# Performance work log

Measured on AMD Instinct MI355X. Metric: run time of the kernel, lower is better.

Reference implementation:

```python
import jax, jax.numpy as jnp
import numpy as np


def setup_inputs() -> dict:
    key = jax.random.key(0)
    ks = jax.random.split(key, 8)
    B, C, N = 2, 128, 8192
    E, NNZ = 1024, 4096
    return {
        "vertex_feat": jax.random.normal(ks[0], (B, C, N), dtype=jnp.float32),
        "edge_feat": jax.random.normal(ks[1], (B, C, E), dtype=jnp.float32),
        "edge_weight": jax.random.uniform(ks[2], (E,), dtype=jnp.float32),
        "incidence": jax.random.randint(ks[3], (2, NNZ), 0, E, dtype=jnp.int64),
        "inv_edge_degree": jax.random.uniform(ks[4], (E,), dtype=jnp.float32),
        "inv_vertex_degree": jax.random.uniform(ks[5], (N,), dtype=jnp.float32),
        "edge_scale": jnp.ones((1,), dtype=jnp.float32),
        "knn_k": 20,
    }


def _knn_edge_aggregate(vertex_feat, knn_k):
    # vertex_feat: [B, C, N]
    B, C, N = vertex_feat.shape
    x = vertex_feat
    xx = jnp.sum(x * x, axis=1)                      # [B, N]
    inner = -2.0 * jnp.einsum("bcn,bcm->bnm", x, x)  # [B, N, N]
    dist = xx[:, :, None] + inner + xx[:, None, :]    # [B, N, N]
    # topk of -dist, drop self (nearest)
    _, idx = jax.lax.top_k(-dist, knn_k + 1)          # [B, N, k+1]
    idx = idx[:, :, 1:]                               # [B, N, k]
    vf = jnp.transpose(x, (0, 2, 1))                  # [B, N, C]
    # batched gather of neighbor features -> [B, N, k, C]
    neighbor = vf[jnp.arange(B)[:, None, None], idx]
    rel = neighbor - vf[:, :, None, :]                # relative positions
    m = jnp.max(rel, axis=2)                          # [B, N, C]
    return x + jnp.transpose(m, (0, 2, 1))            # [B, C, N]


def reference(vertex_feat, edge_feat, edge_weight, incidence,
              inv_edge_degree, inv_vertex_degree, edge_scale, knn_k):
    # use_knn=True path of feature_aggregation_layer.forward;
    # edge_* / incidence / degree args are unused in this branch.
    return _knn_edge_aggregate(vertex_feat, knn_k)
```

## Files before the change

kernel.cpp:

```cpp
#include <hip/hip_runtime.h>

#define NQ 8192
#define CD 128
#define NB 2
#define KNN 20
#define QB 32
#define TB 128
#define LDC 136
#define LDSD 132
#define LOSCALE 4096.0f
#define LOINV (1.0f / 4096.0f)

using f16x8 = __attribute__((ext_vector_type(8))) _Float16;
using f16x2 = __attribute__((ext_vector_type(2))) _Float16;
using f32x4 = __attribute__((ext_vector_type(4))) float;

__global__ __launch_bounds__(256) void k_transpose(const float* __restrict__ x,
                                                   _Float16* __restrict__ vhi,
                                                   _Float16* __restrict__ vlo) {
  __shared__ float tile[32][33];
  int bid = blockIdx.x;
  int ctile = bid & 3;
  int ntile = (bid >> 2) & 255;
  int b = bid >> 10;
  int c0 = ctile << 5, n0 = ntile << 5;
  int tx = threadIdx.x & 31, ty = threadIdx.x >> 5;
  const float* xb = x + (size_t)b * CD * NQ;
  _Float16* hb = vhi + (size_t)b * NQ * CD;
  _Float16* lb = vlo + (size_t)b * NQ * CD;
#pragma unroll
  for (int i = 0; i < 4; ++i) {
    int c = ty + (i << 3);
    tile[c][tx] = xb[(size_t)(c0 + c) * NQ + n0 + tx];
  }
  __syncthreads();
#pragma unroll
  for (int i = 0; i < 4; ++i) {
    int n = ty + (i << 3);
    float v = tile[tx][n];
    _Float16 h = (_Float16)v;
    float hf = (float)h;
    _Float16 l = (_Float16)((v - hf) * LOSCALE);
    size_t o = (size_t)(n0 + n) * CD + c0 + tx;
    hb[o] = h;
    lb[o] = l;
  }
}

__global__ __launch_bounds__(256) void k_xx(const float* __restrict__ x,
                                            float* __restrict__ xx) {
  int n = blockIdx.x * 256 + threadIdx.x;
  int b = blockIdx.y;
  const float* xb = x + (size_t)b * CD * NQ + n;
  float s = 0.f;
#pragma unroll
  for (int c = 0; c < CD; ++c) {
    float v = xb[(size_t)c * NQ];
    s += v * v;
  }
  xx[(size_t)b * NQ + n] = s;
}

__global__ __launch_bounds__(512, 4) void k_knn(const _Float16* __restrict__ vhi,
                                                const _Float16* __restrict__ vlo,
                                                const float* __restrict__ xx,
                                                int* __restrict__ idxout) {
  __shared__ char ubuf[TB * LDC * 2];
  __shared__ _Float16 clo[TB][LDC];
  __shared__ float xq[QB];
  __shared__ float xc[TB];
  auto chi = (_Float16(*)[LDC])ubuf;
  auto sd = (float(*)[LDSD])ubuf;

  const int t = threadIdx.x;
  const int blk = blockIdx.x;
  const int b = blk >> 8;
  const int q0 = (blk & 255) * QB;
  const _Float16* hb = vhi + (size_t)b * NQ * CD;
  const _Float16* lb = vlo + (size_t)b * NQ * CD;
  const float* xb = xx + (size_t)b * NQ;

  const int lane = t & 63, w = t >> 6;

  if (t < QB) xq[t] = xb[q0 + t];

  f16x8 ahi[2][4], alo[2][4];
  {
    const int kof = (lane >> 4) * 8;
#pragma unroll
    for (int s = 0; s < 2; ++s) {
      int row = q0 + 16 * s + (lane & 15);
      const _Float16* hrow = hb + (size_t)row * CD + kof;
      const _Float16* lrow = lb + (size_t)row * CD + kof;
#pragma unroll
      for (int ks = 0; ks < 4; ++ks) {
        ahi[s][ks] = *(const f16x8*)(hrow + ks * 32);
        alo[s][ks] = *(const f16x8*)(lrow + ks * 32);
      }
    }
  }

  float ed[4]; int ei[4]; float tau[4];
#pragma unroll
  for (int u = 0; u < 4; ++u) { ed[u] = 3.0e38f; ei[u] = 0; tau[u] = 3.0e38f; }

  auto insert1 = [&](float& edu, int& eiu, float d, int ci) {
    float sh = __shfl_up(edu, 1);
    int shi = __shfl_up(eiu, 1);
    bool cprev = (lane > 0) && (d < sh);
    bool ccur = d < edu;
    edu = ccur ? (cprev ? sh : d) : edu;
    eiu = ccur ? (cprev ? shi : ci) : eiu;
  };

  for (int tile = 0; tile < NQ / TB; ++tile) {
    const int c0 = tile * TB;
    __syncthreads();

#pragma unroll
    for (int i = 0; i < 4; ++i) {
      int e = t + i * 512;
      int r = e >> 4, ch = (e & 15) * 8;
      *(f16x8*)&chi[r][ch] = *(const f16x8*)(hb + (size_t)(c0 + r) * CD + ch);
      *(f16x8*)&clo[r][ch] = *(const f16x8*)(lb + (size_t)(c0 + r) * CD + ch);
    }
    if (t < TB) xc[t] = xb[c0 + t];
    __syncthreads();

    f32x4 accA[2], accB[2];
#pragma unroll
    for (int s = 0; s < 2; ++s) {
      accA[s] = (f32x4){0.f, 0.f, 0.f, 0.f};
      accB[s] = (f32x4){0.f, 0.f, 0.f, 0.f};
    }
    const int kof = (lane >> 4) * 8;
    const int cme = 16 * w + (lane & 15);
#pragma unroll
    for (int ks = 0; ks < 4; ++ks) {
      f16x8 bhi = *(const f16x8*)&chi[cme][ks * 32 + kof];
      f16x8 blo = *(const f16x8*)&clo[cme][ks * 32 + kof];
#pragma unroll
      for (int s = 0; s < 2; ++s) {
        accA[s] = __builtin_amdgcn_mfma_f32_16x16x32_f16(ahi[s][ks], bhi, accA[s], 0, 0, 0);
        accB[s] = __builtin_amdgcn_mfma_f32_16x16x32_f16(ahi[s][ks], blo, accB[s], 0, 0, 0);
        accB[s] = __builtin_amdgcn_mfma_f32_16x16x32_f16(alo[s][ks], bhi, accB[s], 0, 0, 0);
      }
    }

    float dv[2][4];
    {
      float xcv = xc[cme];
#pragma unroll
      for (int s = 0; s < 2; ++s) {
#pragma unroll
        for (int r = 0; r < 4; ++r) {
          int qrow = 16 * s + (lane >> 4) * 4 + r;
          float dot = accA[s][r] + accB[s][r] * LOINV;
          float tmp = xq[qrow] + (-2.0f * dot);
          dv[s][r] = tmp + xcv;
        }
      }
    }
    __syncthreads();
#pragma unroll
    for (int s = 0; s < 2; ++s) {
#pragma unroll
      for (int r = 0; r < 4; ++r) {
        int qrow = 16 * s + (lane >> 4) * 4 + r;
        sd[qrow][cme] = dv[s][r];
      }
    }
    __syncthreads();

#pragma unroll
    for (int u = 0; u < 4; ++u) {
      int q = 4 * w + u;
      int qg = q0 + q;
      float d0 = sd[q][lane];
      float d1 = sd[q][64 + lane];
      int cnt = 0;
      unsigned long long m0 = __ballot(d0 < tau[u] && (c0 + lane) != qg);
      while (m0) {
        int l = __builtin_ctzll(m0); m0 &= m0 - 1;
        float d = __shfl(d0, l);
        if (d < tau[u]) {
          insert1(ed[u], ei[u], d, c0 + l);
          if ((++cnt & 7) == 0) tau[u] = __shfl(ed[u], 19);
        }
      }
      tau[u] = __shfl(ed[u], 19);
      unsigned long long m1 = __ballot(d1 < tau[u] && (c0 + 64 + lane) != qg);
      while (m1) {
        int l = __builtin_ctzll(m1); m1 &= m1 - 1;
        float d = __shfl(d1, l);
        if (d < tau[u]) {
          insert1(ed[u], ei[u], d, c0 + 64 + l);
          if ((++cnt & 7) == 0) tau[u] = __shfl(ed[u], 19);
        }
      }
      tau[u] = __shfl(ed[u], 19);
    }
  }

  if (lane < KNN) {
#pragma unroll
    for (int u = 0; u < 4; ++u)
      idxout[(size_t)(b * NQ + q0 + 4 * w + u) * KNN + lane] = ei[u];
  }
}

__global__ __launch_bounds__(256) void k_gather(const _Float16* __restrict__ vhi,
                                                const _Float16* __restrict__ vlo,
                                                const int* __restrict__ idx,
                                                float* __restrict__ out) {
  __shared__ float tile[CD][65];
  int blk = blockIdx.x;
  int b = blk >> 7;
  int n0 = (blk & 127) * 64;
  int w = threadIdx.x >> 6, lane = threadIdx.x & 63;
  const _Float16* hb = vhi + (size_t)b * NQ * CD;
  const _Float16* lb = vlo + (size_t)b * NQ * CD;
  for (int s = 0; s < 16; ++s) {
    int nl = w * 16 + s;
    const int* id = idx + (size_t)(b * NQ + n0 + nl) * KNN;
    float ma = -3.0e38f, mb = -3.0e38f;
#pragma unroll
    for (int j = 0; j < KNN; ++j) {
      size_t ro = (size_t)id[j] * CD + 2 * lane;
      f16x2 h = *(const f16x2*)(hb + ro);
      f16x2 l = *(const f16x2*)(lb + ro);
      ma = fmaxf(ma, fmaf((float)l[0], LOINV, (float)h[0]));
      mb = fmaxf(mb, fmaf((float)l[1], LOINV, (float)h[1]));
    }
    tile[2 * lane][nl] = ma;
    tile[2 * lane + 1][nl] = mb;
  }
  __syncthreads();
  float* ob = out + (size_t)b * CD * NQ;
  for (int i = 0; i < 32; ++i) {
    int e = threadIdx.x + i * 256;
    int c = e >> 6, j = e & 63;
    ob[(size_t)c * NQ + n0 + j] = tile[c][j];
  }
}

extern "C" void kernel_launch(void* const* d_in, const int* in_sizes, int n_in,
                              void* d_out, int out_size, void* d_ws, size_t ws_size,
                              hipStream_t stream) {
  const float* x = (const float*)d_in[0];
  size_t velems = (size_t)NB * NQ * CD;
  _Float16* vhi = (_Float16*)d_ws;
  _Float16* vlo = vhi + velems;
  float* xx = (float*)((char*)d_ws + velems * 4);
  int* idx = (int*)((char*)xx + (size_t)NB * NQ * 4);
  float* out = (float*)d_out;

  k_transpose<<<dim3(NB * 256 * 4), dim3(256), 0, stream>>>(x, vhi, vlo);
  k_xx<<<dim3(NQ / 256, NB), dim3(256), 0, stream>>>(x, xx);
  k_knn<<<dim3(NB * NQ / QB), dim3(512), 0, stream>>>(vhi, vlo, xx, idx);
  k_gather<<<dim3(NB * NQ / 64), dim3(256), 0, stream>>>(vhi, vlo, idx, out);
}
```

Measured before the change: 435.3 us.

## Filter kNN candidates with single fp16 MFMA, then rescore top-32 exactly

Replaces the three-MFMA hi/lo split distance with one fp16 MFMA per tile and keeps 32 candidates per query instead of 20. After the scan, the 32 candidates are rescored with hi+lo reconstructed dot products and bitonic-sorted to emit the exact top 20. Query block size is halved to 16 and the low-part LDS tile is removed. This cuts matrix work and LDS traffic, but adds more insertions and a refinement step, and risks missing true neighbours outside the fp16 top 32.

```diff
diff --git a/kernel.cpp b/kernel.cpp
--- a/kernel.cpp
+++ b/kernel.cpp
@@ -4,10 +4,11 @@
 #define CD 128
 #define NB 2
 #define KNN 20
-#define QB 32
+#define QB 16
 #define TB 128
 #define LDC 136
 #define LDSD 132
+#define NSEL 32
 #define LOSCALE 4096.0f
 #define LOINV (1.0f / 4096.0f)
 
@@ -66,7 +67,6 @@
                                                 const float* __restrict__ xx,
                                                 int* __restrict__ idxout) {
   __shared__ char ubuf[TB * LDC * 2];
-  __shared__ _Float16 clo[TB][LDC];
   __shared__ float xq[QB];
   __shared__ float xc[TB];
   auto chi = (_Float16(*)[LDC])ubuf;
@@ -74,8 +74,8 @@
 
   const int t = threadIdx.x;
   const int blk = blockIdx.x;
-  const int b = blk >> 8;
-  const int q0 = (blk & 255) * QB;
+  const int b = blk >> 9;
+  const int q0 = (blk & 511) * QB;
   const _Float16* hb = vhi + (size_t)b * NQ * CD;
   const _Float16* lb = vlo + (size_t)b * NQ * CD;
   const float* xb = xx + (size_t)b * NQ;
@@ -84,25 +84,18 @@
 
   if (t < QB) xq[t] = xb[q0 + t];
 
-  f16x8 ahi[2][4], alo[2][4];
+  f16x8 ahi[4];
   {
-    const int kof = (lane >> 4) * 8;
-#pragma unroll
-    for (int s = 0; s < 2; ++s) {
-      int row = q0 + 16 * s + (lane & 15);
-      const _Float16* hrow = hb + (size_t)row * CD + kof;
-      const _Float16* lrow = lb + (size_t)row * CD + kof;
-#pragma unroll
-      for (int ks = 0; ks < 4; ++ks) {
-        ahi[s][ks] = *(const f16x8*)(hrow + ks * 32);
-        alo[s][ks] = *(const f16x8*)(lrow + ks * 32);
-      }
-    }
-  }
-
-  float ed[4]; int ei[4]; float tau[4];
-#pragma unroll
-  for (int u = 0; u < 4; ++u) { ed[u] = 3.0e38f; ei[u] = 0; tau[u] = 3.0e38f; }
+    int row = q0 + (lane & 15);
+    int kof = (lane >> 4) * 8;
+    const _Float16* hrow = hb + (size_t)row * CD + kof;
+#pragma unroll
+    for (int ks = 0; ks < 4; ++ks) ahi[ks] = *(const f16x8*)(hrow + ks * 32);
+  }
+
+  float ed[2]; int ei[2]; float tau[2];
+#pragma unroll
+  for (int u = 0; u < 2; ++u) { ed[u] = 3.0e38f; ei[u] = 0; tau[u] = 3.0e38f; }
 
   auto insert1 = [&](float& edu, int& eiu, float d, int ci) {
     float sh = __shfl_up(edu, 1);
@@ -122,59 +115,39 @@
       int e = t + i * 512;
       int r = e >> 4, ch = (e & 15) * 8;
       *(f16x8*)&chi[r][ch] = *(const f16x8*)(hb + (size_t)(c0 + r) * CD + ch);
-      *(f16x8*)&clo[r][ch] = *(const f16x8*)(lb + (size_t)(c0 + r) * CD + ch);
     }
     if (t < TB) xc[t] = xb[c0 + t];
     __syncthreads();
 
-    f32x4 accA[2], accB[2];
-#pragma unroll
-    for (int s = 0; s < 2; ++s) {
-      accA[s] = (f32x4){0.f, 0.f, 0.f, 0.f};
-      accB[s] = (f32x4){0.f, 0.f, 0.f, 0.f};
-    }
+    f32x4 acc = (f32x4){0.f, 0.f, 0.f, 0.f};
     const int kof = (lane >> 4) * 8;
     const int cme = 16 * w + (lane & 15);
 #pragma unroll
     for (int ks = 0; ks < 4; ++ks) {
       f16x8 bhi = *(const f16x8*)&chi[cme][ks * 32 + kof];
-      f16x8 blo = *(const f16x8*)&clo[cme][ks * 32 + kof];
-#pragma unroll
-      for (int s = 0; s < 2; ++s) {
-        accA[s] = __builtin_amdgcn_mfma_f32_16x16x32_f16(ahi[s][ks], bhi, accA[s], 0, 0, 0);
-        accB[s] = __builtin_amdgcn_mfma_f32_16x16x32_f16(ahi[s][ks], blo, accB[s], 0, 0, 0);
-        accB[s] = __builtin_amdgcn_mfma_f32_16x16x32_f16(alo[s][ks], bhi, accB[s], 0, 0, 0);
-      }
-    }
-
-    float dv[2][4];
+      acc = __builtin_amdgcn_mfma_f32_16x16x32_f16(ahi[ks], bhi, acc, 0, 0, 0);
+    }
+
+    float dv[4];
     {
       float xcv = xc[cme];
 #pragma unroll
-      for (int s = 0; s < 2; ++s) {
-#pragma unroll
-        for (int r = 0; r < 4; ++r) {
-          int qrow = 16 * s + (lane >> 4) * 4 + r;
-          float dot = accA[s][r] + accB[s][r] * LOINV;
-          float tmp = xq[qrow] + (-2.0f * dot);
-          dv[s][r] = tmp + xcv;
-        }
-      }
-    }
-    __syncthreads();
-#pragma unroll
-    for (int s = 0; s < 2; ++s) {
-#pragma unroll
       for (int r = 0; r < 4; ++r) {
-        int qrow = 16 * s + (lane >> 4) * 4 + r;
-        sd[qrow][cme] = dv[s][r];
-      }
-    }
-    __syncthreads();
-
-#pragma unroll
-    for (int u = 0; u < 4; ++u) {
-      int q = 4 * w + u;
+        int qrow = (lane >> 4) * 4 + r;
+        dv[r] = xq[qrow] + xcv - 2.0f * acc[r];
+      }
+    }
+    __syncthreads();
+#pragma unroll
+    for (int r = 0; r < 4; ++r) {
+      int qrow = (lane >> 4) * 4 + r;
+      sd[qrow][cme] = dv[r];
+    }
+    __syncthreads();
+
+#pragma unroll
+    for (int u = 0; u < 2; ++u) {
+      int q = 2 * w + u;
       int qg = q0 + q;
       float d0 = sd[q][lane];
       float d1 = sd[q][64 + lane];
@@ -185,27 +158,68 @@
         float d = __shfl(d0, l);
         if (d < tau[u]) {
           insert1(ed[u], ei[u], d, c0 + l);
-          if ((++cnt & 7) == 0) tau[u] = __shfl(ed[u], 19);
+          if ((++cnt & 7) == 0) tau[u] = __shfl(ed[u], NSEL - 1);
         }
       }
-      tau[u] = __shfl(ed[u], 19);
+      tau[u] = __shfl(ed[u], NSEL - 1);
       unsigned long long m1 = __ballot(d1 < tau[u] && (c0 + 64 + lane) != qg);
       while (m1) {
         int l = __builtin_ctzll(m1); m1 &= m1 - 1;
         float d = __shfl(d1, l);
         if (d < tau[u]) {
           insert1(ed[u], ei[u], d, c0 + 64 + l);
-          if ((++cnt & 7) == 0) tau[u] = __shfl(ed[u], 19);
+          if ((++cnt & 7) == 0) tau[u] = __shfl(ed[u], NSEL - 1);
         }
       }
-      tau[u] = __shfl(ed[u], 19);
-    }
-  }
-
-  if (lane < KNN) {
-#pragma unroll
-    for (int u = 0; u < 4; ++u)
-      idxout[(size_t)(b * NQ + q0 + 4 * w + u) * KNN + lane] = ei[u];
+      tau[u] = __shfl(ed[u], NSEL - 1);
+    }
+  }
+
+  {
+    const int r32 = lane & 31;
+    const int u = lane >> 5;
+    float d1s = __shfl(ed[1], r32);
+    int i1s = __shfl(ei[1], r32);
+    int ci = (u == 0) ? ei[0] : i1s;
+    (void)d1s;
+
+    const int ql = 2 * w + u;
+    const _Float16* qh = hb + (size_t)(q0 + ql) * CD;
+    const _Float16* qlo = lb + (size_t)(q0 + ql) * CD;
+    const _Float16* ch = hb + (size_t)ci * CD;
+    const _Float16* cl = lb + (size_t)ci * CD;
+
+    float dot = 0.f;
+#pragma unroll
+    for (int kc = 0; kc < CD / 8; ++kc) {
+      f16x8 ah = *(const f16x8*)(qh + kc * 8);
+      f16x8 al = *(const f16x8*)(qlo + kc * 8);
+      f16x8 bh = *(const f16x8*)(ch + kc * 8);
+      f16x8 bl = *(const f16x8*)(cl + kc * 8);
+#pragma unroll
+      for (int e = 0; e < 8; ++e) {
+        float qv = fmaf((float)al[e], LOINV, (float)ah[e]);
+        float cv = fmaf((float)bl[e], LOINV, (float)bh[e]);
+        dot = fmaf(qv, cv, dot);
+      }
+    }
+    float dex = (xq[ql] + (-2.0f * dot)) + xb[ci];
+
+#pragma unroll
+    for (int k = 2; k <= 32; k <<= 1) {
+#pragma unroll
+      for (int j = k >> 1; j >= 1; j >>= 1) {
+        float od = __shfl_xor(dex, j);
+        int oi = __shfl_xor(ci, j);
+        bool lower = !(r32 & j);
+        bool up = ((r32 & k) == 0) || (k == 32);
+        bool tt = (od < dex) || (od == dex && oi < ci);
+        if (tt == (lower == up)) { dex = od; ci = oi; }
+      }
+    }
+
+    if (r32 < KNN)
+      idxout[(size_t)(b * NQ + q0 + ql) * KNN + r32] = ci;
   }
 }
 
```

After: 537.9 us. +23.6%, slower.
